# Optimization experiments

Hardware: AMD Instinct MI355X
Metric: run time of the kernel (lower is better)

## Reference

```python
import jax, jax.numpy as jnp
import numpy as np

B, H, W = 8, 160, 180
PHASES = 3
DELTA = 0.01
GAMMA = 1.0


def _conv(a, k):
    return jax.lax.conv_general_dilated(a, k, (1, 1), 'SAME',
                                        dimension_numbers=('NCHW', 'OIHW', 'NCHW'))


def _cconv(xr, xi, kr, ki):
    # complex conv via 4 real convs: (xr+i xi) * (kr+i ki)
    return _conv(xr, kr) - _conv(xi, ki), _conv(xr, ki) + _conv(xi, kr)


def _t(k):
    # conv_transpose2d(stride=1, pad=1, 3x3) == conv2d with swapped in/out channels and spatially flipped kernel
    return jnp.flip(jnp.swapaxes(k, 0, 1), axis=(2, 3))


def _cconvT(xr, xi, kr, ki):
    return _cconv(xr, xi, _t(kr), _t(ki))


def _act(x):
    # eq. (33): smoothed ReLU; quadratic inside |x| <= delta
    return jnp.where(jnp.abs(x) > DELTA, jax.nn.relu(x),
                     x * x / (4 * DELTA) + 0.5 * x + DELTA / 4)


def _act_der(x):
    return jnp.where(jnp.abs(x) > DELTA, (x > 0).astype(x.dtype),
                     x / (2 * DELTA) + 0.5)


def _grad_r(xc, convs, thr):
    # gradient of smoothed L2-channel-norm regularizer (grad_r_x1 / grad_r_x2)
    xr = jnp.real(xc).reshape(-1, 1, H, W)
    xi = jnp.imag(xc).reshape(-1, 1, H, W)
    acts = []
    ar, ai = xr, xi
    for kr, ki in convs[:3]:
        pr, pi = _cconv(ar, ai, kr, ki)
        ar, ai = _act(pr), _act(pi)
        acts.append((ar, ai))
    w4r, w4i = _cconv(ar, ai, *convs[3])
    norm = jnp.sqrt(jnp.sum(w4r * w4r + w4i * w4i, axis=1, keepdims=True))
    I1 = (norm > thr).astype(w4r.dtype)
    denom = jnp.maximum(norm, 1e-12)  # F.normalize eps
    gr = I1 * (w4r / denom) + (1 - I1) * (w4r / thr)
    gi = I1 * (w4i / denom) + (1 - I1) * (w4i / thr)
    gr, gi = _cconvT(gr, gi, *convs[3])
    for j in (2, 1, 0):
        # NOTE: faithful to source — derivative evaluated at the ACTIVATED values, complex multiply
        dr, di = _act_der(acts[j][0]), _act_der(acts[j][1])
        gr, gi = gr * dr - gi * di, gr * di + gi * dr
        gr, gi = _cconvT(gr, gi, *convs[j])
    return (gr + 1j * gi).reshape(-1, H, W)


def _grad_f(xc, kc, mask):
    # F^H( M o (M o F x - k) ): mriAdjointOp(mriForwardOp(x,m) - k, m)
    return jnp.fft.ifft2((jnp.fft.fft2(xc) * mask - kc) * mask)


def _forward(x1, x2, k1, k2, mask, convsA, convsB, thr1, thr2, a1, a2, b1, b2):
    to_c = lambda a: a[:, 0] + 1j * a[:, 1]
    x1c, x2c, k1c, k2c = to_c(x1), to_c(x2), to_c(k1), to_c(k2)
    for i in range(PHASES):
        x1c = x1c - a1[i] * _grad_f(x1c, k1c, mask) - b1[i] * _grad_r(x1c, convsA, thr1[0] * GAMMA)
        x2c = x2c - a2[i] * _grad_f(x2c, k2c, mask) - b2[i] * _grad_r(x2c, convsB, thr2[0] * GAMMA)
    return jnp.stack([jnp.real(x1c), jnp.imag(x1c), jnp.real(x2c), jnp.imag(x2c)], axis=1)


def setup_inputs() -> dict:
    key = jax.random.key(0)
    ks = jax.random.split(key, 32)
    d = {}
    d['x1'] = jax.random.normal(ks[0], (B, 2, H, W), jnp.float32)
    d['x2'] = jax.random.normal(ks[1], (B, 2, H, W), jnp.float32)
    d['k1'] = jax.random.normal(ks[2], (B, 2, H, W), jnp.float32)
    d['k2'] = jax.random.normal(ks[3], (B, 2, H, W), jnp.float32)
    d['mask'] = jax.random.uniform(ks[4], (H, W), jnp.float32)
    conv_names = ['conv1r', 'conv1i', 'conv2r', 'conv2i', 'conv3r', 'conv3i', 'conv4r', 'conv4i',
                  'conv1r_', 'conv1i_', 'conv2r_', 'conv2i_', 'conv3r_', 'conv3i_', 'conv4r_', 'conv4i_']
    for j, name in enumerate(conv_names):
        cin = 1 if name.startswith('conv1') else 32
        d[name] = 0.06 * jax.random.normal(ks[5 + j], (32, cin, 3, 3), jnp.float32)  # ~xavier
    d['soft_thr1'] = jnp.full((1,), 0.01, jnp.float32)
    d['soft_thr2'] = jnp.full((1,), 0.01, jnp.float32)
    d['alphas1'] = jnp.full((PHASES,), 0.5, jnp.float32)
    d['alphas2'] = jnp.full((PHASES,), 0.5, jnp.float32)
    d['betas1'] = jnp.full((PHASES,), 0.1, jnp.float32)
    d['betas2'] = jnp.full((PHASES,), 0.1, jnp.float32)
    return d


def reference(x1, x2, k1, k2, mask,
              conv1r, conv1i, conv2r, conv2i, conv3r, conv3i, conv4r, conv4i,
              conv1r_, conv1i_, conv2r_, conv2i_, conv3r_, conv3i_, conv4r_, conv4i_,
              soft_thr1, soft_thr2, alphas1, alphas2, betas1, betas2):
    convsA = [(conv1r, conv1i), (conv2r, conv2i), (conv3r, conv3i), (conv4r, conv4i)]
    convsB = [(conv1r_, conv1i_), (conv2r_, conv2i_), (conv3r_, conv3i_), (conv4r_, conv4i_)]
    return _forward(x1, x2, k1, k2, mask, convsA, convsB,
                    soft_thr1, soft_thr2, alphas1, alphas2, betas1, betas2)
```

## Files before the change

kernel.cpp:

```cpp
#include <hip/hip_runtime.h>
#include <math.h>

#define HH 160
#define WW 180
#define HWSZ (HH*WW)
#define BB 8
#define BB2 16
#define P1 ((size_t)BB*HWSZ)
#define PE2 ((size_t)BB2*32*HWSZ)

#define NCONV 3840

typedef unsigned short u16;
typedef unsigned long long ull;
typedef __attribute__((ext_vector_type(8))) short short8;
typedef __attribute__((ext_vector_type(2))) unsigned long long ull2;
typedef __attribute__((ext_vector_type(4))) float floatx4;

struct Ptrs16 { const float* p[16]; };

__device__ __forceinline__ u16 f2b(float f) {
  unsigned u = __builtin_bit_cast(unsigned, f);
  unsigned r = (u + 0x7fffu + ((u >> 16) & 1u)) >> 16;
  return (u16)r;
}
__device__ __forceinline__ float b2f(u16 h) {
  return __builtin_bit_cast(float, ((unsigned)h) << 16);
}

__device__ __forceinline__ float actf(float x) {
  float q = x*x*25.0f + 0.5f*x + 0.0025f;
  float r = fmaxf(x, 0.0f);
  return (fabsf(x) > 0.01f) ? r : q;
}
__device__ __forceinline__ float actdf(float x) {
  float q = x*50.0f + 0.5f;
  float r = (x > 0.0f) ? 1.0f : 0.0f;
  return (fabsf(x) > 0.01f) ? r : q;
}

__global__ __launch_bounds__(256)
void setup_all(Ptrs16 ps, u16* __restrict__ wp0,
               const float* __restrict__ x1, const float* __restrict__ x2,
               float* __restrict__ xall,
               const float* __restrict__ k1, const float* __restrict__ k2,
               const float* __restrict__ mask, float2* __restrict__ t1,
               float2* __restrict__ EWf, float2* __restrict__ EWi,
               float2* __restrict__ EHf, float2* __restrict__ EHi)
{
  const int id = blockIdx.x, tid = threadIdx.x;
  if (id < 127) {
    int idx = id*256 + tid; if (idx >= WW*WW) return;
    int r = idx / WW, c = idx - r*WW;
    long mm = ((long)r * (long)c) % WW;
    double a = 2.0 * 3.14159265358979323846 * (double)mm / (double)WW;
    double cs = cos(a), sn = sin(a);
    EWf[idx] = make_float2((float)cs, (float)(-sn));
    EWi[idx] = make_float2((float)(cs/WW), (float)(sn/WW));
  } else if (id < 227) {
    int idx = (id-127)*256 + tid; if (idx >= HH*HH) return;
    int r = idx / HH, c = idx - r*HH;
    long mm = ((long)r * (long)c) % HH;
    double a = 2.0 * 3.14159265358979323846 * (double)mm / (double)HH;
    double cs = cos(a), sn = sin(a);
    EHf[idx] = make_float2((float)cs, (float)(-sn));
    EHi[idx] = make_float2((float)(cs/HH), (float)(sn/HH));
  } else if (id < 659) {
    const int rIdx[12] = {2,4,6,6,4,2,10,12,14,14,12,10};
    const int bwdF[12] = {0,0,0,1,1,1,0,0,0,1,1,1};
    int pb = id - 227;
    int slot = pb / 36;
    int idx = (pb % 36)*256 + tid;
    if (idx >= 9*32*32) return;
    const float* wr = ps.p[rIdx[slot]];
    const float* wi = ps.p[rIdx[slot]+1];
    u16* dst = wp0 + (size_t)slot*18432;
    int tap = idx >> 10; int rem = idx & 1023; int o = rem >> 5; int c = rem & 31;
    int s = bwdF[slot] ? ((c*32 + o)*9 + (8 - tap)) : ((o*32 + c)*9 + tap);
    int nt = o >> 4, m = o & 15;
    size_t base = (((size_t)tap*2 + nt)*2*16 + (size_t)m)*32 + c;
    dst[base]       = f2b(wr[s]);
    dst[base + 512] = f2b(wi[s]);
  } else if (id < 2459) {
    int i = (id-659)*256 + tid; if (i >= (int)(2*P1)) return;
    int branch = i >= (int)P1;
    int ii = i - branch*(int)P1;
    int b = ii / HWSZ, p = ii - b*HWSZ;
    const float* src = branch ? x2 : x1;
    size_t dst = (size_t)branch*2*P1 + (size_t)b*HWSZ + p;
    xall[dst]      = src[(size_t)b*2*HWSZ + p];
    xall[P1 + dst] = src[(size_t)b*2*HWSZ + HWSZ + p];
  } else {
    int i = (id-2459)*256 + tid; if (i >= (int)(2*P1)) return;
    int branch = i >= (int)P1;
    int ii = i - branch*(int)P1;
    int b = ii / HWSZ, p = ii - b*HWSZ;
    const float* k = branch ? k2 : k1;
    float m = mask[p];
    t1[i] = make_float2(m * k[(size_t)b*2*HWSZ + p], m * k[(size_t)b*2*HWSZ + HWSZ + p]);
  }
}

template<int MODE, int EXTRA>
__global__ __launch_bounds__(256)
void conv_mfma(const u16* __restrict__ inb, const u16* __restrict__ wbA,
               const u16* __restrict__ wbB, u16* __restrict__ outb,
               const u16* __restrict__ derb,
               const float* __restrict__ thrA, const float* __restrict__ thrB,
               const float* __restrict__ xall, float2* __restrict__ t1,
               const float2* __restrict__ EWf, const float2* __restrict__ EHf,
               const float2* __restrict__ EHi, const float* __restrict__ mask)
{
  __shared__ alignas(16) u16 stg[2*6*34*36];
  const int id = blockIdx.x, tid = threadIdx.x;

  if (EXTRA == 1 && id >= NCONV) {
    int j = id - NCONV;
    int v = tid; if (v >= WW) return;
    int b2 = j / HH, h = j - b2*HH;
    int branch = b2 >> 3, img = b2 & 7;
    const float* rowR = xall + (size_t)branch*2*P1 + (size_t)img*HWSZ + (size_t)h*WW;
    const float* rowI = rowR + P1;
    float ar = 0.f, ai = 0.f;
    for (int w = 0; w < WW; ++w) {
      float sr = rowR[w], si = rowI[w];
      float2 m = EWf[w*WW + v];
      ar += sr*m.x - si*m.y;
      ai += sr*m.y + si*m.x;
    }
    t1[(size_t)j*WW + v] = make_float2(ar, ai);
    return;
  }
  if (EXTRA == 2 && id >= NCONV) {
    int j = id - NCONV;
    int b = j / WW, v = j - b*WW;
    float2* cbA = (float2*)stg;
    float2* cbB = ((float2*)stg) + HH;
    if (tid < HH) cbA[tid] = t1[((size_t)(b*HH) + tid)*WW + v];
    __syncthreads();
    if (tid < HH) {
      int u = tid;
      float ar = 0.f, ai = 0.f;
      for (int h = 0; h < HH; ++h) {
        float2 m = EHf[u*HH + h];
        float2 s = cbA[h];
        ar += s.x*m.x - s.y*m.y;
        ai += s.x*m.y + s.y*m.x;
      }
      float mk = mask[u*WW + v]; float mm = mk*mk;
      cbB[u] = make_float2(ar*mm, ai*mm);
    }
    __syncthreads();
    if (tid < HH) {
      int u2 = tid;
      float ar = 0.f, ai = 0.f;
      for (int u = 0; u < HH; ++u) {
        float2 m = EHi[u2*HH + u];
        float2 s = cbB[u];
        ar += s.x*m.x - s.y*m.y;
        ai += s.x*m.y + s.y*m.x;
      }
      t1[((size_t)(b*HH) + u2)*WW + v] = make_float2(ar, ai);
    }
    return;
  }

  const int lane = tid & 63, wv = tid >> 6;
  const int x0 = (id % 6) * 32;
  const int y0 = ((id / 6) % 40) * 4;
  const int b  = id / 240;
  const u16* wb = (b < BB) ? wbA : wbB;
  constexpr int PL = 6*34*36;
  const int m = lane & 15, q = lane >> 4;

  for (int j = tid; j < 1632; j += 256) {
    int prow = j / 136; int rem = j - prow*136;
    int col = rem >> 2, chq = rem & 3;
    int plane = prow / 6, row = prow - plane*6;
    int gy = y0 - 1 + row, gx = x0 - 1 + col;
    ull v0 = 0, v1 = 0;
    if (gy >= 0 && gy < HH && gx >= 0 && gx < WW) {
      const ull* src = (const ull*)(inb + (size_t)plane*PE2
                                    + (((size_t)b*HH + gy)*WW + gx)*32 + chq*8);
      v0 = src[0]; v1 = src[1];
    }
    ull* dst = (ull*)&stg[((size_t)prow*34 + col)*36 + chq*8];
    dst[0] = v0; dst[1] = v1;
  }
  __syncthreads();

  floatx4 accr[2][2], acci[2][2];
#pragma unroll
  for (int s = 0; s < 2; ++s)
#pragma unroll
    for (int nt = 0; nt < 2; ++nt) {
      accr[s][nt] = (floatx4){0.f,0.f,0.f,0.f};
      acci[s][nt] = (floatx4){0.f,0.f,0.f,0.f};
    }

#pragma unroll
  for (int tap = 0; tap < 9; ++tap) {
    const int ky = tap / 3, kx = tap - ky*3;
    short8 Pr[2], Pi[2];
#pragma unroll
    for (int s = 0; s < 2; ++s) {
      int cu = ((wv + ky)*34 + (s*16 + m + kx))*36 + q*8;
      const ull* pR = (const ull*)&stg[cu];
      const ull* pI = (const ull*)&stg[cu + PL];
      ull2 vr; vr.x = pR[0]; vr.y = pR[1];
      ull2 vi; vi.x = pI[0]; vi.y = pI[1];
      Pr[s] = __builtin_bit_cast(short8, vr);
      Pi[s] = __builtin_bit_cast(short8, vi);
    }
#pragma unroll
    for (int nt = 0; nt < 2; ++nt) {
      const u16* pw = wb + (size_t)(tap*2 + nt)*1024 + (size_t)m*32 + q*8;
      short8 Wr = *(const short8*)pw;
      short8 Wi = *(const short8*)(pw + 512);
      ull2 wx = __builtin_bit_cast(ull2, Wi);
      wx.x ^= 0x8000800080008000ULL;
      wx.y ^= 0x8000800080008000ULL;
      short8 nWi = __builtin_bit_cast(short8, wx);
#pragma unroll
      for (int s = 0; s < 2; ++s) {
        accr[s][nt] = __builtin_amdgcn_mfma_f32_16x16x32_bf16(Wr,  Pr[s], accr[s][nt], 0, 0, 0);
        accr[s][nt] = __builtin_amdgcn_mfma_f32_16x16x32_bf16(nWi, Pi[s], accr[s][nt], 0, 0, 0);
        acci[s][nt] = __builtin_amdgcn_mfma_f32_16x16x32_bf16(Wr,  Pi[s], acci[s][nt], 0, 0, 0);
        acci[s][nt] = __builtin_amdgcn_mfma_f32_16x16x32_bf16(Wi,  Pr[s], acci[s][nt], 0, 0, 0);
      }
    }
  }

  const int y = y0 + wv;
#pragma unroll
  for (int s = 0; s < 2; ++s) {
    int x = x0 + s*16 + m;
    bool ok = (x < WW);
    float invn = 1.0f;
    if constexpr (MODE == 3) {
      float ss = 0.f;
#pragma unroll
      for (int nt = 0; nt < 2; ++nt)
#pragma unroll
        for (int r = 0; r < 4; ++r)
          ss += accr[s][nt][r]*accr[s][nt][r] + acci[s][nt][r]*acci[s][nt][r];
      ss += __shfl_xor(ss, 16, 64);
      ss += __shfl_xor(ss, 32, 64);
      float thr = (b < BB ? thrA : thrB)[0];
      invn = 1.0f / fmaxf(sqrtf(ss), thr);
    }
    size_t pxbase = (((size_t)b*HH + y)*WW + x)*32;
#pragma unroll
    for (int nt = 0; nt < 2; ++nt) {
      size_t gb = pxbase + nt*16 + q*4;
      ull dR = 0, dI = 0;
      if constexpr (MODE == 2) {
        if (ok) { dR = *(const ull*)(derb + gb); dI = *(const ull*)(derb + PE2 + gb); }
      }
      ull vR = 0, vI = 0;
#pragma unroll
      for (int r = 0; r < 4; ++r) {
        float pr = accr[s][nt][r], pi = acci[s][nt][r];
        if constexpr (MODE == 1) { pr = actf(pr); pi = actf(pi); }
        if constexpr (MODE == 3) { pr *= invn; pi *= invn; }
        if constexpr (MODE == 2) {
          float dr = actdf(b2f((u16)(dR >> (16*r))));
          float di = actdf(b2f((u16)(dI >> (16*r))));
          float nr = pr*dr - pi*di;
          pi = pr*di + pi*dr; pr = nr;
        }
        vR |= (ull)f2b(pr) << (16*r);
        vI |= (ull)f2b(pi) << (16*r);
      }
      if (ok) {
        *(ull*)(outb + gb)       = vR;
        *(ull*)(outb + PE2 + gb) = vI;
      }
    }
  }
}

__global__ __launch_bounds__(256)
void l1fwd(const float* __restrict__ xall,
           const float* __restrict__ wrA, const float* __restrict__ wiA,
           const float* __restrict__ wrB, const float* __restrict__ wiB,
           u16* __restrict__ outb)
{
  __shared__ float hR[10][12], hI[10][12];
  __shared__ float wt[9][32][2];
  const int tid = threadIdx.x;
  const int og = tid & 3, px = tid >> 2;
  const int lx = px & 7, ly = px >> 3;
  const int x0 = blockIdx.x*8, y0 = blockIdx.y*8, b = blockIdx.z;
  const int branch = b >> 3, img = b & 7;
  const float* wr = branch ? wrB : wrA;
  const float* wi = branch ? wiB : wiA;
  const float* xp = xall + (size_t)branch*2*P1 + (size_t)img*HWSZ;

  for (int j = tid; j < 576; j += 256) {
    int tap = j >> 6; int rem = j & 63; int o = rem >> 1, ri = rem & 1;
    wt[tap][o][ri] = ri ? wi[o*9+tap] : wr[o*9+tap];
  }
  for (int j = tid; j < 200; j += 256) {
    int plane = j / 100; int pos = j - plane*100;
    int yy = pos / 10, xx = pos - yy*10;
    int gy = y0 - 1 + yy, gx = x0 - 1 + xx;
    float v = 0.f;
    if (gy >= 0 && gy < HH && gx >= 0 && gx < WW)
      v = xp[(size_t)plane*P1 + (size_t)gy*WW + gx];
    (plane ? hI : hR)[yy][xx] = v;
  }
  __syncthreads();

  float accR[8], accI[8];
#pragma unroll
  for (int o = 0; o < 8; ++o) { accR[o] = 0.f; accI[o] = 0.f; }
#pragma unroll
  for (int tap = 0; tap < 9; ++tap) {
    int ky = tap/3, kx = tap - ky*3;
    float ar = hR[ly+ky][lx+kx], ai = hI[ly+ky][lx+kx];
#pragma unroll
    for (int o = 0; o < 8; ++o) {
      float wrv = wt[tap][og*8+o][0], wiv = wt[tap][og*8+o][1];
      accR[o] += ar*wrv - ai*wiv;
      accI[o] += ar*wiv + ai*wrv;
    }
  }
  int gx = x0 + lx, gy = y0 + ly;
  if (gx < WW) {
    size_t base = (((size_t)b*HH + gy)*WW + gx)*32 + og*8;
    ull* dR = (ull*)(outb + base);
    ull* dI = (ull*)(outb + PE2 + base);
#pragma unroll
    for (int k = 0; k < 2; ++k) {
      ull vR = 0, vI = 0;
#pragma unroll
      for (int t = 0; t < 4; ++t) {
        vR |= (ull)f2b(actf(accR[k*4+t])) << (16*t);
        vI |= (ull)f2b(actf(accI[k*4+t])) << (16*t);
      }
      dR[k] = vR; dI[k] = vI;
    }
  }
}

__global__ __launch_bounds__(256)
void l1bwd(const u16* __restrict__ gb,
           const float* __restrict__ wrA, const float* __restrict__ wiA,
           const float* __restrict__ wrB, const float* __restrict__ wiB,
           float* __restrict__ outp)
{
  __shared__ alignas(16) u16 stg[2*100*32];
  __shared__ float wt[32][9][2];
  const int tid = threadIdx.x;
  const int cg = tid & 3, px = tid >> 2;
  const int lx = px & 7, ly = px >> 3;
  const int x0 = blockIdx.x*8, y0 = blockIdx.y*8, b = blockIdx.z;
  const int branch = b >> 3, img = b & 7;
  const float* wr = branch ? wrB : wrA;
  const float* wi = branch ? wiB : wiA;

  for (int j = tid; j < 576; j += 256) {
    int c = j / 18; int rem = j - c*18; int tap = rem >> 1, ri = rem & 1;
    wt[c][tap][ri] = (ri ? wi : wr)[c*9 + (8-tap)];
  }
  for (int j = tid; j < 800; j += 256) {
    int plane = j / 400; int rem = j - plane*400;
    int pos = rem >> 2, chq = rem & 3;
    int yy = pos / 10, xx = pos - yy*10;
    int gy = y0 - 1 + yy, gx = x0 - 1 + xx;
    ull v0 = 0, v1 = 0;
    if (gy >= 0 && gy < HH && gx >= 0 && gx < WW) {
      const ull* src = (const ull*)(gb + (size_t)plane*PE2
                                    + (((size_t)b*HH + gy)*WW + gx)*32 + chq*8);
      v0 = src[0]; v1 = src[1];
    }
    ull* dst = (ull*)&stg[((size_t)plane*100 + pos)*32 + chq*8];
    dst[0] = v0; dst[1] = v1;
  }
  __syncthreads();

  float gr = 0.f, gi = 0.f;
#pragma unroll
  for (int tap = 0; tap < 9; ++tap) {
    int ky = tap/3, kx = tap - ky*3;
    int pos = (ly+ky)*10 + (lx+kx);
    const ull* pR = (const ull*)&stg[(size_t)pos*32 + cg*8];
    const ull* pI = (const ull*)&stg[(100 + (size_t)pos)*32 + cg*8];
    ull r0 = pR[0], r1 = pR[1], i0 = pI[0], i1 = pI[1];
#pragma unroll
    for (int t = 0; t < 4; ++t) {
      int c = cg*8 + t;
      float ar = b2f((u16)(r0 >> (16*t))), ai = b2f((u16)(i0 >> (16*t)));
      float wrv = wt[c][tap][0], wiv = wt[c][tap][1];
      gr += ar*wrv - ai*wiv;
      gi += ar*wiv + ai*wrv;
    }
#pragma unroll
    for (int t = 0; t < 4; ++t) {
      int c = cg*8 + 4 + t;
      float ar = b2f((u16)(r1 >> (16*t))), ai = b2f((u16)(i1 >> (16*t)));
      float wrv = wt[c][tap][0], wiv = wt[c][tap][1];
      gr += ar*wrv - ai*wiv;
      gi += ar*wiv + ai*wrv;
    }
  }
  gr += __shfl_xor(gr, 1, 64); gr += __shfl_xor(gr, 2, 64);
  gi += __shfl_xor(gi, 1, 64); gi += __shfl_xor(gi, 2, 64);

  int gx = x0 + lx, gy = y0 + ly;
  if (cg == 0 && gx < WW) {
    size_t o2 = (size_t)branch*2*P1 + (size_t)img*HWSZ + (size_t)gy*WW + gx;
    outp[o2]      = gr;
    outp[P1 + o2] = gi;
  }
}

__global__ void dft_col_c(const float2* __restrict__ in, float2* __restrict__ out,
                          const float2* __restrict__ M) {
  int bu = blockIdx.x;
  int v = threadIdx.x; if (v >= WW) return;
  int b = bu / HH, u = bu - b*HH;
  const float2* base = in + (size_t)b*HWSZ;
  float ar = 0.f, ai = 0.f;
  for (int h = 0; h < HH; ++h) {
    float2 m = M[u*HH + h];
    float2 s = base[(size_t)h*WW + v];
    ar += s.x*m.x - s.y*m.y;
    ai += s.x*m.y + s.y*m.x;
  }
  out[(size_t)bu*WW + v] = make_float2(ar, ai);
}

__global__ void dft_row_c(const float2* __restrict__ in, float2* __restrict__ out,
                          const float2* __restrict__ M) {
  int bh = blockIdx.x;
  int v = threadIdx.x; if (v >= WW) return;
  const float2* row = in + (size_t)bh*WW;
  float ar = 0.f, ai = 0.f;
  for (int w = 0; w < WW; ++w) {
    float2 s = row[w];
    float2 m = M[w*WW + v];
    ar += s.x*m.x - s.y*m.y;
    ai += s.x*m.y + s.y*m.x;
  }
  out[(size_t)bh*WW + v] = make_float2(ar, ai);
}

__global__ void dft_row_update(const float2* __restrict__ in, const float2* __restrict__ M,
                               const float2* __restrict__ ctall, const float* __restrict__ grp,
                               float* __restrict__ xall,
                               const float* __restrict__ al1, const float* __restrict__ al2,
                               const float* __restrict__ be1, const float* __restrict__ be2,
                               int phase) {
  int bh = blockIdx.x;
  int v = threadIdx.x; if (v >= WW) return;
  int b2 = bh / HH, h = bh - b2*HH;
  int branch = b2 >> 3, img = b2 & 7;
  const float2* row = in + (size_t)bh*WW;
  float ar = 0.f, ai = 0.f;
  for (int w = 0; w < WW; ++w) {
    float2 s = row[w];
    float2 m = M[w*WW + v];
    ar += s.x*m.x - s.y*m.y;
    ai += s.x*m.y + s.y*m.x;
  }
  float2 ct = ctall[(size_t)bh*WW + v];
  float a   = (branch ? al2 : al1)[phase];
  float bet = (branch ? be2 : be1)[phase];
  size_t xo = (size_t)branch*2*P1 + (size_t)img*HWSZ + (size_t)h*WW + v;
  xall[xo]      -= a*(ar - ct.x) + bet*grp[xo];
  xall[P1 + xo] -= a*(ai - ct.y) + bet*grp[P1 + xo];
}

__global__ void pack_kernel(const float* __restrict__ xall, float* __restrict__ out) {
  int i = blockIdx.x*256 + threadIdx.x;
  if (i >= (int)P1) return;
  int b = i / HWSZ, p = i - b*HWSZ;
  size_t ob = (size_t)b*4*HWSZ;
  size_t x1o = (size_t)b*HWSZ + p;
  size_t x2o = 2*P1 + x1o;
  out[ob + p]          = xall[x1o];
  out[ob + HWSZ + p]   = xall[P1 + x1o];
  out[ob + 2*HWSZ + p] = xall[x2o];
  out[ob + 3*HWSZ + p] = xall[P1 + x2o];
}

extern "C" void kernel_launch(void* const* d_in, const int* in_sizes, int n_in,
                              void* d_out, int out_size, void* d_ws, size_t ws_size,
                              hipStream_t stream) {
  (void)in_sizes; (void)n_in; (void)out_size; (void)ws_size;
  const float* x1in = (const float*)d_in[0];
  const float* x2in = (const float*)d_in[1];
  const float* k1   = (const float*)d_in[2];
  const float* k2   = (const float*)d_in[3];
  const float* mask = (const float*)d_in[4];
  Ptrs16 cw;
  for (int i = 0; i < 16; ++i) cw.p[i] = (const float*)d_in[5+i];
  const float* thr1 = (const float*)d_in[21];
  const float* thr2 = (const float*)d_in[22];
  const float* al1  = (const float*)d_in[23];
  const float* al2  = (const float*)d_in[24];
  const float* be1  = (const float*)d_in[25];
  const float* be2  = (const float*)d_in[26];
  float* out = (float*)d_out;

  u16* U = (u16*)d_ws;
  size_t uoff = 0;
  auto alloc_u = [&](size_t n){ u16* p = U + uoff; uoff += (n + 15) & ~(size_t)15; return p; };
  u16* act1 = alloc_u(2*PE2);
  u16* act2 = alloc_u(2*PE2);
  u16* act3 = alloc_u(2*PE2);
  u16* w4b  = alloc_u(2*PE2);
  u16* wp0  = alloc_u(12*18432);

  float* F = (float*)(U + uoff);
  size_t off = 0;
  auto alloc_f = [&](size_t n){ float* p = F + off; off += (n + 3) & ~(size_t)3; return p; };
  float*  xall = alloc_f(4*P1);
  float*  grp  = alloc_f(4*P1);
  float2* t1   = (float2*)alloc_f(4*P1);
  float2* t2   = (float2*)alloc_f(4*P1);
  float2* ctall= (float2*)alloc_f(4*P1);
  float2* EWf  = (float2*)alloc_f(2*(size_t)WW*WW);
  float2* EWi  = (float2*)alloc_f(2*(size_t)WW*WW);
  float2* EHf  = (float2*)alloc_f(2*(size_t)HH*HH);
  float2* EHi  = (float2*)alloc_f(2*(size_t)HH*HH);

  const dim3 LG(23, 20, BB2);
  const int NP1 = (int)((P1 + 255)/256);
  const int DFTG = BB2*HH;
  const int DFTB = 192;

  setup_all<<<4259, 256, 0, stream>>>(cw, wp0, x1in, x2in, xall, k1, k2, mask, t1,
                                      EWf, EWi, EHf, EHi);
  dft_col_c<<<DFTG, DFTB, 0, stream>>>(t1, t2, EHi);
  dft_row_c<<<DFTG, DFTB, 0, stream>>>(t2, ctall, EWi);

  u16* WA[6]; u16* WB[6];
  for (int i = 0; i < 6; ++i) { WA[i] = wp0 + (size_t)i*18432; WB[i] = wp0 + (size_t)(6+i)*18432; }

  for (int ph = 0; ph < 3; ++ph) {
    l1fwd<<<LG, 256, 0, stream>>>(xall, cw.p[0], cw.p[1], cw.p[8], cw.p[9], act1);
    conv_mfma<1,1><<<NCONV + 2560, 256, 0, stream>>>(act1, WA[0], WB[0], act2, nullptr,
        nullptr, nullptr, xall, t1, EWf, EHf, EHi, mask);
    conv_mfma<1,2><<<NCONV + BB2*WW, 256, 0, stream>>>(act2, WA[1], WB[1], act3, nullptr,
        nullptr, nullptr, xall, t1, EWf, EHf, EHi, mask);
    conv_mfma<3,0><<<NCONV, 256, 0, stream>>>(act3, WA[2], WB[2], w4b, nullptr,
        thr1, thr2, xall, t1, EWf, EHf, EHi, mask);
    conv_mfma<2,0><<<NCONV, 256, 0, stream>>>(w4b,  WA[3], WB[3], act3, act3,
        nullptr, nullptr, xall, t1, EWf, EHf, EHi, mask);
    conv_mfma<2,0><<<NCONV, 256, 0, stream>>>(act3, WA[4], WB[4], act2, act2,
        nullptr, nullptr, xall, t1, EWf, EHf, EHi, mask);
    conv_mfma<2,0><<<NCONV, 256, 0, stream>>>(act2, WA[5], WB[5], act1, act1,
        nullptr, nullptr, xall, t1, EWf, EHf, EHi, mask);
    l1bwd<<<LG, 256, 0, stream>>>(act1, cw.p[0], cw.p[1], cw.p[8], cw.p[9], grp);
    dft_row_update<<<DFTG, DFTB, 0, stream>>>(t1, EWi, ctall, grp, xall,
                                              al1, al2, be1, be2, ph);
  }

  pack_kernel<<<NP1, 256, 0, stream>>>(xall, out);
}
```

Baseline: 2.157 ms.

## Tile conv over 8 rows with halo reuse and split DFT work into separate kernels

Each conv block now covers 8 output rows in two passes of 4. After the first pass it loads only the two new halo rows into a rotating shared-memory ring, which cuts redundant halo loads and halves the number of blocks. The DFT row and column work that was folded into the conv launches as extra blocks now runs in dedicated kernels after l1bwd, adding two launches and removing the overlap with the conv. The larger tile uses more LDS per block, and the grid shrinks to 1920 blocks, which may lower occupancy.

```diff
diff --git a/kernel.cpp b/kernel.cpp
--- a/kernel.cpp
+++ b/kernel.cpp
@@ -8,8 +8,6 @@
 #define BB2 16
 #define P1 ((size_t)BB*HWSZ)
 #define PE2 ((size_t)BB2*32*HWSZ)
-
-#define NCONV 3840
 
 typedef unsigned short u16;
 typedef unsigned long long ull;
@@ -101,82 +99,25 @@
   }
 }
 
-template<int MODE, int EXTRA>
+template<int MODE>
 __global__ __launch_bounds__(256)
 void conv_mfma(const u16* __restrict__ inb, const u16* __restrict__ wbA,
                const u16* __restrict__ wbB, u16* __restrict__ outb,
                const u16* __restrict__ derb,
-               const float* __restrict__ thrA, const float* __restrict__ thrB,
-               const float* __restrict__ xall, float2* __restrict__ t1,
-               const float2* __restrict__ EWf, const float2* __restrict__ EHf,
-               const float2* __restrict__ EHi, const float* __restrict__ mask)
+               const float* __restrict__ thrA, const float* __restrict__ thrB)
 {
-  __shared__ alignas(16) u16 stg[2*6*34*36];
-  const int id = blockIdx.x, tid = threadIdx.x;
-
-  if (EXTRA == 1 && id >= NCONV) {
-    int j = id - NCONV;
-    int v = tid; if (v >= WW) return;
-    int b2 = j / HH, h = j - b2*HH;
-    int branch = b2 >> 3, img = b2 & 7;
-    const float* rowR = xall + (size_t)branch*2*P1 + (size_t)img*HWSZ + (size_t)h*WW;
-    const float* rowI = rowR + P1;
-    float ar = 0.f, ai = 0.f;
-    for (int w = 0; w < WW; ++w) {
-      float sr = rowR[w], si = rowI[w];
-      float2 m = EWf[w*WW + v];
-      ar += sr*m.x - si*m.y;
-      ai += sr*m.y + si*m.x;
-    }
-    t1[(size_t)j*WW + v] = make_float2(ar, ai);
-    return;
-  }
-  if (EXTRA == 2 && id >= NCONV) {
-    int j = id - NCONV;
-    int b = j / WW, v = j - b*WW;
-    float2* cbA = (float2*)stg;
-    float2* cbB = ((float2*)stg) + HH;
-    if (tid < HH) cbA[tid] = t1[((size_t)(b*HH) + tid)*WW + v];
-    __syncthreads();
-    if (tid < HH) {
-      int u = tid;
-      float ar = 0.f, ai = 0.f;
-      for (int h = 0; h < HH; ++h) {
-        float2 m = EHf[u*HH + h];
-        float2 s = cbA[h];
-        ar += s.x*m.x - s.y*m.y;
-        ai += s.x*m.y + s.y*m.x;
-      }
-      float mk = mask[u*WW + v]; float mm = mk*mk;
-      cbB[u] = make_float2(ar*mm, ai*mm);
-    }
-    __syncthreads();
-    if (tid < HH) {
-      int u2 = tid;
-      float ar = 0.f, ai = 0.f;
-      for (int u = 0; u < HH; ++u) {
-        float2 m = EHi[u2*HH + u];
-        float2 s = cbB[u];
-        ar += s.x*m.x - s.y*m.y;
-        ai += s.x*m.y + s.y*m.x;
-      }
-      t1[((size_t)(b*HH) + u2)*WW + v] = make_float2(ar, ai);
-    }
-    return;
-  }
-
+  constexpr int PL = 8*34*36;
+  __shared__ alignas(16) u16 stg[2*PL];
+  const int tid = threadIdx.x;
   const int lane = tid & 63, wv = tid >> 6;
-  const int x0 = (id % 6) * 32;
-  const int y0 = ((id / 6) % 40) * 4;
-  const int b  = id / 240;
+  const int x0 = blockIdx.x * 32, y0 = blockIdx.y * 8, b = blockIdx.z;
   const u16* wb = (b < BB) ? wbA : wbB;
-  constexpr int PL = 6*34*36;
   const int m = lane & 15, q = lane >> 4;
 
-  for (int j = tid; j < 1632; j += 256) {
+  for (int j = tid; j < 2176; j += 256) {
     int prow = j / 136; int rem = j - prow*136;
     int col = rem >> 2, chq = rem & 3;
-    int plane = prow / 6, row = prow - plane*6;
+    int plane = prow >> 3, row = prow & 7;
     int gy = y0 - 1 + row, gx = x0 - 1 + col;
     ull v0 = 0, v1 = 0;
     if (gy >= 0 && gy < HH && gx >= 0 && gx < WW) {
@@ -184,98 +125,120 @@
                                     + (((size_t)b*HH + gy)*WW + gx)*32 + chq*8);
       v0 = src[0]; v1 = src[1];
     }
-    ull* dst = (ull*)&stg[((size_t)prow*34 + col)*36 + chq*8];
+    ull* dst = (ull*)&stg[((size_t)(plane*8 + row)*34 + col)*36 + chq*8];
     dst[0] = v0; dst[1] = v1;
   }
   __syncthreads();
 
-  floatx4 accr[2][2], acci[2][2];
-#pragma unroll
-  for (int s = 0; s < 2; ++s)
-#pragma unroll
-    for (int nt = 0; nt < 2; ++nt) {
-      accr[s][nt] = (floatx4){0.f,0.f,0.f,0.f};
-      acci[s][nt] = (floatx4){0.f,0.f,0.f,0.f};
-    }
-
-#pragma unroll
-  for (int tap = 0; tap < 9; ++tap) {
-    const int ky = tap / 3, kx = tap - ky*3;
-    short8 Pr[2], Pi[2];
+  for (int t = 0; t < 2; ++t) {
+    floatx4 accr[2][2], acci[2][2];
+#pragma unroll
+    for (int s = 0; s < 2; ++s)
+#pragma unroll
+      for (int nt = 0; nt < 2; ++nt) {
+        accr[s][nt] = (floatx4){0.f,0.f,0.f,0.f};
+        acci[s][nt] = (floatx4){0.f,0.f,0.f,0.f};
+      }
+
+#pragma unroll
+    for (int tap = 0; tap < 9; ++tap) {
+      const int ky = tap / 3, kx = tap - ky*3;
+      const int rs = (4*t + wv + ky) & 7;
+      short8 Pr[2], Pi[2];
+#pragma unroll
+      for (int s = 0; s < 2; ++s) {
+        int cu = (rs*34 + (s*16 + m + kx))*36 + q*8;
+        const ull* pR = (const ull*)&stg[cu];
+        const ull* pI = (const ull*)&stg[cu + PL];
+        ull2 vr; vr.x = pR[0]; vr.y = pR[1];
+        ull2 vi; vi.x = pI[0]; vi.y = pI[1];
+        Pr[s] = __builtin_bit_cast(short8, vr);
+        Pi[s] = __builtin_bit_cast(short8, vi);
+      }
+#pragma unroll
+      for (int nt = 0; nt < 2; ++nt) {
+        const u16* pw = wb + (size_t)(tap*2 + nt)*1024 + (size_t)m*32 + q*8;
+        short8 Wr = *(const short8*)pw;
+        short8 Wi = *(const short8*)(pw + 512);
+        ull2 wx = __builtin_bit_cast(ull2, Wi);
+        wx.x ^= 0x8000800080008000ULL;
+        wx.y ^= 0x8000800080008000ULL;
+        short8 nWi = __builtin_bit_cast(short8, wx);
+#pragma unroll
+        for (int s = 0; s < 2; ++s) {
+          accr[s][nt] = __builtin_amdgcn_mfma_f32_16x16x32_bf16(Wr,  Pr[s], accr[s][nt], 0, 0, 0);
+          accr[s][nt] = __builtin_amdgcn_mfma_f32_16x16x32_bf16(nWi, Pi[s], accr[s][nt], 0, 0, 0);
+          acci[s][nt] = __builtin_amdgcn_mfma_f32_16x16x32_bf16(Wr,  Pi[s], acci[s][nt], 0, 0, 0);
+          acci[s][nt] = __builtin_amdgcn_mfma_f32_16x16x32_bf16(Wi,  Pr[s], acci[s][nt], 0, 0, 0);
+        }
+      }
+    }
+
+    const int y = y0 + 4*t + wv;
 #pragma unroll
     for (int s = 0; s < 2; ++s) {
-      int cu = ((wv + ky)*34 + (s*16 + m + kx))*36 + q*8;
-      const ull* pR = (const ull*)&stg[cu];
-      const ull* pI = (const ull*)&stg[cu + PL];
-      ull2 vr; vr.x = pR[0]; vr.y = pR[1];
-      ull2 vi; vi.x = pI[0]; vi.y = pI[1];
-      Pr[s] = __builtin_bit_cast(short8, vr);
-      Pi[s] = __builtin_bit_cast(short8, vi);
-    }
-#pragma unroll
-    for (int nt = 0; nt < 2; ++nt) {
-      const u16* pw = wb + (size_t)(tap*2 + nt)*1024 + (size_t)m*32 + q*8;
-      short8 Wr = *(const short8*)pw;
-      short8 Wi = *(const short8*)(pw + 512);
-      ull2 wx = __builtin_bit_cast(ull2, Wi);
-      wx.x ^= 0x8000800080008000ULL;
-      wx.y ^= 0x8000800080008000ULL;
-      short8 nWi = __builtin_bit_cast(short8, wx);
-#pragma unroll
-      for (int s = 0; s < 2; ++s) {
-        accr[s][nt] = __builtin_amdgcn_mfma_f32_16x16x32_bf16(Wr,  Pr[s], accr[s][nt], 0, 0, 0);
-        accr[s][nt] = __builtin_amdgcn_mfma_f32_16x16x32_bf16(nWi, Pi[s], accr[s][nt], 0, 0, 0);
-        acci[s][nt] = __builtin_amdgcn_mfma_f32_16x16x32_bf16(Wr,  Pi[s], acci[s][nt], 0, 0, 0);
-        acci[s][nt] = __builtin_amdgcn_mfma_f32_16x16x32_bf16(Wi,  Pr[s], acci[s][nt], 0, 0, 0);
-      }
-    }
-  }
-
-  const int y = y0 + wv;
-#pragma unroll
-  for (int s = 0; s < 2; ++s) {
-    int x = x0 + s*16 + m;
-    bool ok = (x < WW);
-    float invn = 1.0f;
-    if constexpr (MODE == 3) {
-      float ss = 0.f;
-#pragma unroll
-      for (int nt = 0; nt < 2; ++nt)
-#pragma unroll
-        for (int r = 0; r < 4; ++r)
-          ss += accr[s][nt][r]*accr[s][nt][r] + acci[s][nt][r]*acci[s][nt][r];
-      ss += __shfl_xor(ss, 16, 64);
-      ss += __shfl_xor(ss, 32, 64);
-      float thr = (b < BB ? thrA : thrB)[0];
-      invn = 1.0f / fmaxf(sqrtf(ss), thr);
-    }
-    size_t pxbase = (((size_t)b*HH + y)*WW + x)*32;
-#pragma unroll
-    for (int nt = 0; nt < 2; ++nt) {
-      size_t gb = pxbase + nt*16 + q*4;
-      ull dR = 0, dI = 0;
-      if constexpr (MODE == 2) {
-        if (ok) { dR = *(const ull*)(derb + gb); dI = *(const ull*)(derb + PE2 + gb); }
-      }
-      ull vR = 0, vI = 0;
-#pragma unroll
-      for (int r = 0; r < 4; ++r) {
-        float pr = accr[s][nt][r], pi = acci[s][nt][r];
-        if constexpr (MODE == 1) { pr = actf(pr); pi = actf(pi); }
-        if constexpr (MODE == 3) { pr *= invn; pi *= invn; }
+      int x = x0 + s*16 + m;
+      bool ok = (x < WW);
+      float invn = 1.0f;
+      if constexpr (MODE == 3) {
+        float ss = 0.f;
+#pragma unroll
+        for (int nt = 0; nt < 2; ++nt)
+#pragma unroll
+          for (int r = 0; r < 4; ++r)
+            ss += accr[s][nt][r]*accr[s][nt][r] + acci[s][nt][r]*acci[s][nt][r];
+        ss += __shfl_xor(ss, 16, 64);
+        ss += __shfl_xor(ss, 32, 64);
+        float thr = (b < BB ? thrA : thrB)[0];
+        invn = 1.0f / fmaxf(sqrtf(ss), thr);
+      }
+      size_t pxbase = (((size_t)b*HH + y)*WW + x)*32;
+#pragma unroll
+      for (int nt = 0; nt < 2; ++nt) {
+        size_t gb = pxbase + nt*16 + q*4;
+        ull dR = 0, dI = 0;
         if constexpr (MODE == 2) {
-          float dr = actdf(b2f((u16)(dR >> (16*r))));
-          float di = actdf(b2f((u16)(dI >> (16*r))));
-          float nr = pr*dr - pi*di;
-          pi = pr*di + pi*dr; pr = nr;
+          if (ok) { dR = *(const ull*)(derb + gb); dI = *(const ull*)(derb + PE2 + gb); }
         }
-        vR |= (ull)f2b(pr) << (16*r);
-        vI |= (ull)f2b(pi) << (16*r);
-      }
-      if (ok) {
-        *(ull*)(outb + gb)       = vR;
-        *(ull*)(outb + PE2 + gb) = vI;
-      }
+        ull vR = 0, vI = 0;
+#pragma unroll
+        for (int r = 0; r < 4; ++r) {
+          float pr = accr[s][nt][r], pi = acci[s][nt][r];
+          if constexpr (MODE == 1) { pr = actf(pr); pi = actf(pi); }
+          if constexpr (MODE == 3) { pr *= invn; pi *= invn; }
+          if constexpr (MODE == 2) {
+            float dr = actdf(b2f((u16)(dR >> (16*r))));
+            float di = actdf(b2f((u16)(dI >> (16*r))));
+            float nr = pr*dr - pi*di;
+            pi = pr*di + pi*dr; pr = nr;
+          }
+          vR |= (ull)f2b(pr) << (16*r);
+          vI |= (ull)f2b(pi) << (16*r);
+        }
+        if (ok) {
+          *(ull*)(outb + gb)       = vR;
+          *(ull*)(outb + PE2 + gb) = vI;
+        }
+      }
+    }
+
+    if (t == 0) {
+      __syncthreads();
+      for (int j = tid; j < 544; j += 256) {
+        int prow = j / 136; int rem = j - prow*136;
+        int col = rem >> 2, chq = rem & 3;
+        int plane = prow >> 1, rr = prow & 1;
+        int gy = y0 + 7 + rr, gx = x0 - 1 + col;
+        ull v0 = 0, v1 = 0;
+        if (gy < HH && gx >= 0 && gx < WW) {
+          const ull* src = (const ull*)(inb + (size_t)plane*PE2
+                                        + (((size_t)b*HH + gy)*WW + gx)*32 + chq*8);
+          v0 = src[0]; v1 = src[1];
+        }
+        ull* dst = (ull*)&stg[((size_t)(plane*8 + rr)*34 + col)*36 + chq*8];
+        dst[0] = v0; dst[1] = v1;
+      }
+      __syncthreads();
     }
   }
 }
@@ -445,6 +408,59 @@
     ai += s.x*m.y + s.y*m.x;
   }
   out[(size_t)bh*WW + v] = make_float2(ar, ai);
+}
+
+__global__ void dft_row_planes(const float* __restrict__ xall,
+                               float2* __restrict__ out, const float2* __restrict__ M) {
+  int bh = blockIdx.x;
+  int v = threadIdx.x; if (v >= WW) return;
+  int b2 = bh / HH, h = bh - b2*HH;
+  int branch = b2 >> 3, img = b2 & 7;
+  const float* rowR = xall + (size_t)branch*2*P1 + (size_t)img*HWSZ + (size_t)h*WW;
+  const float* rowI = rowR + P1;
+  float ar = 0.f, ai = 0.f;
+  for (int w = 0; w < WW; ++w) {
+    float sr = rowR[w], si = rowI[w];
+    float2 m = M[w*WW + v];
+    ar += sr*m.x - si*m.y;
+    ai += sr*m.y + si*m.x;
+  }
+  out[(size_t)bh*WW + v] = make_float2(ar, ai);
+}
+
+__global__ __launch_bounds__(192)
+void dft_mid(float2* __restrict__ t1, const float2* __restrict__ EHf,
+             const float2* __restrict__ EHi, const float* __restrict__ mask) {
+  __shared__ float2 cbA[HH], cbB[HH];
+  int j = blockIdx.x;
+  int b = j / WW, v = j - b*WW;
+  int tid = threadIdx.x;
+  if (tid < HH) cbA[tid] = t1[((size_t)(b*HH) + tid)*WW + v];
+  __syncthreads();
+  if (tid < HH) {
+    int u = tid;
+    float ar = 0.f, ai = 0.f;
+    for (int h = 0; h < HH; ++h) {
+      float2 m = EHf[u*HH + h];
+      float2 s = cbA[h];
+      ar += s.x*m.x - s.y*m.y;
+      ai += s.x*m.y + s.y*m.x;
+    }
+    float mk = mask[u*WW + v]; float mm = mk*mk;
+    cbB[u] = make_float2(ar*mm, ai*mm);
+  }
+  __syncthreads();
+  if (tid < HH) {
+    int u2 = tid;
+    float ar = 0.f, ai = 0.f;
+    for (int u = 0; u < HH; ++u) {
+      float2 m = EHi[u2*HH + u];
+      float2 s = cbB[u];
+      ar += s.x*m.x - s.y*m.y;
+      ai += s.x*m.y + s.y*m.x;
+    }
+    t1[((size_t)(b*HH) + u2)*WW + v] = make_float2(ar, ai);
+  }
 }
 
 __global__ void dft_row_update(const float2* __restrict__ in, const float2* __restrict__ M,
@@ -527,6 +543,7 @@
   float2* EHf  = (float2*)alloc_f(2*(size_t)HH*HH);
   float2* EHi  = (float2*)alloc_f(2*(size_t)HH*HH);
 
+  const dim3 MG(6, 20, BB2);
   const dim3 LG(23, 20, BB2);
   const int NP1 = (int)((P1 + 255)/256);
   const int DFTG = BB2*HH;
@@ -542,19 +559,15 @@
 
   for (int ph = 0; ph < 3; ++ph) {
     l1fwd<<<LG, 256, 0, stream>>>(xall, cw.p[0], cw.p[1], cw.p[8], cw.p[9], act1);
-    conv_mfma<1,1><<<NCONV + 2560, 256, 0, stream>>>(act1, WA[0], WB[0], act2, nullptr,
-        nullptr, nullptr, xall, t1, EWf, EHf, EHi, mask);
-    conv_mfma<1,2><<<NCONV + BB2*WW, 256, 0, stream>>>(act2, WA[1], WB[1], act3, nullptr,
-        nullptr, nullptr, xall, t1, EWf, EHf, EHi, mask);
-    conv_mfma<3,0><<<NCONV, 256, 0, stream>>>(act3, WA[2], WB[2], w4b, nullptr,
-        thr1, thr2, xall, t1, EWf, EHf, EHi, mask);
-    conv_mfma<2,0><<<NCONV, 256, 0, stream>>>(w4b,  WA[3], WB[3], act3, act3,
-        nullptr, nullptr, xall, t1, EWf, EHf, EHi, mask);
-    conv_mfma<2,0><<<NCONV, 256, 0, stream>>>(act3, WA[4], WB[4], act2, act2,
-        nullptr, nullptr, xall, t1, EWf, EHf, EHi, mask);
-    conv_mfma<2,0><<<NCONV, 256, 0, stream>>>(act2, WA[5], WB[5], act1, act1,
-        nullptr, nullptr, xall, t1, EWf, EHf, EHi, mask);
+    conv_mfma<1><<<MG, 256, 0, stream>>>(act1, WA[0], WB[0], act2, nullptr, nullptr, nullptr);
+    conv_mfma<1><<<MG, 256, 0, stream>>>(act2, WA[1], WB[1], act3, nullptr, nullptr, nullptr);
+    conv_mfma<3><<<MG, 256, 0, stream>>>(act3, WA[2], WB[2], w4b, nullptr, thr1, thr2);
+    conv_mfma<2><<<MG, 256, 0, stream>>>(w4b,  WA[3], WB[3], act3, act3, nullptr, nullptr);
+    conv_mfma<2><<<MG, 256, 0, stream>>>(act3, WA[4], WB[4], act2, act2, nullptr, nullptr);
+    conv_mfma<2><<<MG, 256, 0, stream>>>(act2, WA[5], WB[5], act1, act1, nullptr, nullptr);
     l1bwd<<<LG, 256, 0, stream>>>(act1, cw.p[0], cw.p[1], cw.p[8], cw.p[9], grp);
+    dft_row_planes<<<DFTG, DFTB, 0, stream>>>(xall, t1, EWf);
+    dft_mid<<<BB2*WW, 192, 0, stream>>>(t1, EHf, EHi, mask);
     dft_row_update<<<DFTG, DFTB, 0, stream>>>(t1, EWi, ctall, grp, xall,
                                               al1, al2, be1, be2, ph);
   }
```

Result: slower. 2.806 ms (+30.1%).
